# Kernel tuning notes

Hardware: AMD Instinct MI355X
Metric: run time of the kernel (lower is better)

The kernel has to match this reference:

```python
import jax, jax.numpy as jnp
import numpy as np

NUM_HEADS = 8
NUM_GROUPS = 32
EMB = 512
EPS = 1e-5


def setup_inputs() -> dict:
    key = jax.random.key(0)
    ks = jax.random.split(key, 12)
    B, C, H, W = 256, EMB, 16, 16
    s = 1.0 / np.sqrt(C)
    x = jax.random.normal(ks[0], (B, C, H, W), dtype=jnp.float32)
    Wq = jax.random.normal(ks[1], (C, EMB), dtype=jnp.float32) * s
    bq = jax.random.normal(ks[2], (EMB,), dtype=jnp.float32) * 0.01
    Wk = jax.random.normal(ks[3], (C, EMB), dtype=jnp.float32) * s
    bk = jax.random.normal(ks[4], (EMB,), dtype=jnp.float32) * 0.01
    Wv = jax.random.normal(ks[5], (C, EMB), dtype=jnp.float32) * s
    bv = jax.random.normal(ks[6], (EMB,), dtype=jnp.float32) * 0.01
    Wf = jax.random.normal(ks[7], (EMB, EMB), dtype=jnp.float32) * s
    bf = jax.random.normal(ks[8], (EMB,), dtype=jnp.float32) * 0.01
    gn_w = jnp.ones((EMB,), dtype=jnp.float32)
    gn_b = jnp.zeros((EMB,), dtype=jnp.float32)
    return {"x": x, "Wq": Wq, "bq": bq, "Wk": Wk, "bk": bk,
            "Wv": Wv, "bv": bv, "Wf": Wf, "bf": bf,
            "gn_w": gn_w, "gn_b": gn_b}


def reference(x, Wq, bq, Wk, bk, Wv, bv, Wf, bf, gn_w, gn_b):
    B, C, H, W = x.shape
    S = H * W
    nh = NUM_HEADS
    dh = EMB // nh
    xs = x.reshape(B, C, S).transpose(0, 2, 1)  # [B, S, C]
    q = (xs @ Wq + bq).reshape(B, S, nh, dh)
    k = (xs @ Wk + bk).reshape(B, S, nh, dh)
    v = (xs @ Wv + bv).reshape(B, S, nh, dh)
    scale = dh ** -0.5
    logits = jnp.einsum('bshd,bthd->bhst', q, k) * scale  # [B, nh, S, S]
    attn = jax.nn.softmax(logits, axis=-1)
    o = jnp.einsum('bhst,bthd->bshd', attn, v).reshape(B, S, EMB)
    o = o @ Wf + bf  # [B, S, EMB]
    y = o.transpose(0, 2, 1).reshape(B, EMB, H, W) + x  # residual
    # GroupNorm over (channels-within-group, H, W)
    G = NUM_GROUPS
    yg = y.reshape(B, G, EMB // G, H, W)
    mu = jnp.mean(yg, axis=(2, 3, 4), keepdims=True)
    var = jnp.var(yg, axis=(2, 3, 4), keepdims=True)
    yn = ((yg - mu) * jax.lax.rsqrt(var + EPS)).reshape(B, EMB, H, W)
    return yn * gn_w.reshape(1, EMB, 1, 1) + gn_b.reshape(1, EMB, 1, 1)
```

## Files before the change

kernel.cpp:

```cpp
#include <hip/hip_runtime.h>
#include <hip/hip_bf16.h>
#include <stdint.h>

#define B_  256
#define C_  512
#define S_  256
#define NH  8
#define DH  64

typedef float f32x4 __attribute__((ext_vector_type(4)));
typedef short s16x8 __attribute__((ext_vector_type(8)));

static __device__ __forceinline__ unsigned short f2bf(float f) {
  union { float f; unsigned u; } v; v.f = f;
  unsigned r = v.u + 0x7FFFu + ((v.u >> 16) & 1u);
  return (unsigned short)(r >> 16);
}

static __device__ __forceinline__ unsigned pk_bf16(float lo, float hi) {
  unsigned r;
  asm("v_cvt_pk_bf16_f32 %0, %1, %2" : "=v"(r) : "v"(lo), "v"(hi));
  return r;
}

static __device__ __forceinline__ void gload_lds16(const void* g, void* l) {
  __builtin_amdgcn_global_load_lds((const __attribute__((address_space(1))) void*)g,
                                   (__attribute__((address_space(3))) void*)l,
                                   16, 0, 0);
}

__global__ __launch_bounds__(256) void prep_w(const float* __restrict__ Wq,
                                              const float* __restrict__ Wk,
                                              const float* __restrict__ Wv,
                                              const float* __restrict__ Wf,
                                              unsigned short* __restrict__ Whead,
                                              unsigned short* __restrict__ Wft) {
  int mat = blockIdx.z;
  const float* src = (mat == 0) ? Wq : (mat == 1) ? Wk : (mat == 2) ? Wv : Wf;
  int n0 = blockIdx.x * 64, c0 = blockIdx.y * 64;
  __shared__ float tile[64][65];
  int t = threadIdx.x;
  int tr = t >> 4;
  int tc = (t & 15) * 4;
#pragma unroll
  for (int i = 0; i < 4; ++i) {
    int c = tr + i * 16;
    float4 v = *(const float4*)&src[(size_t)(c0 + c) * 512 + n0 + tc];
    tile[c][tc + 0] = v.x; tile[c][tc + 1] = v.y;
    tile[c][tc + 2] = v.z; tile[c][tc + 3] = v.w;
  }
  __syncthreads();
  int h = n0 >> 6;
  unsigned short* dst = (mat < 3) ? (Whead + ((size_t)h * 192 + mat * 64) * 512)
                                  : (Wft + (size_t)n0 * 512);
#pragma unroll
  for (int i = 0; i < 4; ++i) {
    int nl = tr + i * 16;
    ushort4 o;
    o.x = f2bf(tile[tc + 0][nl]); o.y = f2bf(tile[tc + 1][nl]);
    o.z = f2bf(tile[tc + 2][nl]); o.w = f2bf(tile[tc + 3][nl]);
    *(ushort4*)&dst[(size_t)nl * 512 + c0 + tc] = o;
  }
}

__global__ __launch_bounds__(256) void prep_x(const float* __restrict__ x,
                                              unsigned short* __restrict__ xs) {
  int b = blockIdx.z, s0 = blockIdx.x * 64, c0 = blockIdx.y * 64;
  __shared__ float tile[64][65];
  int t = threadIdx.x;
  int tr = t >> 4, tc = (t & 15) * 4;
  const float* xb = x + (size_t)b * C_ * S_;
#pragma unroll
  for (int i = 0; i < 4; ++i) {
    int c = tr + i * 16;
    float4 v = *(const float4*)&xb[(size_t)(c0 + c) * S_ + s0 + tc];
    tile[c][tc + 0] = v.x; tile[c][tc + 1] = v.y;
    tile[c][tc + 2] = v.z; tile[c][tc + 3] = v.w;
  }
  __syncthreads();
  unsigned short* xsb = xs + (size_t)b * S_ * C_;
#pragma unroll
  for (int i = 0; i < 4; ++i) {
    int s = tr + i * 16;
    ushort4 o;
    o.x = f2bf(tile[tc + 0][s]); o.y = f2bf(tile[tc + 1][s]);
    o.z = f2bf(tile[tc + 2][s]); o.w = f2bf(tile[tc + 3][s]);
    *(ushort4*)&xsb[(size_t)(s0 + s) * C_ + c0 + tc] = o;
  }
}

#define QKP 68
#define QOFF 0
#define KOFF 34816
#define VOFF 69632
__global__ __launch_bounds__(512) void qkvattn(const unsigned short* __restrict__ xs,
                                               const unsigned short* __restrict__ Whead,
                                               const float* __restrict__ bq,
                                               const float* __restrict__ bk,
                                               const float* __restrict__ bv,
                                               unsigned short* __restrict__ o) {
  __shared__ __align__(16) char lds[114688];
  int bid = blockIdx.x;
  int lin = (bid & 7) * 256 + (bid >> 3);
  int h = lin & 7, b = lin >> 3;
  int t = threadIdx.x, lane = t & 63, w = t >> 6;
  int l15 = lane & 15, l4 = lane >> 4;
  int wr = w >> 2, wc = w & 3;
  const unsigned short* xsb = xs + (size_t)b * S_ * C_;
  const unsigned short* wh  = Whead + (size_t)h * 192 * C_;

#define FSTAGE(kt, p)                                                         \
  {                                                                           \
    _Pragma("unroll")                                                         \
    for (int i = 0; i < 4; ++i) {                                             \
      int ch = i * 512 + t, r = ch >> 3, g = ch & 7;                          \
      int gs = g ^ (r & 7);                                                   \
      gload_lds16(xsb + (size_t)r * C_ + (kt) * 64 + gs * 8,                  \
                  lds + (p) * 57344 + ch * 16);                               \
    }                                                                         \
    _Pragma("unroll")                                                         \
    for (int i = 0; i < 3; ++i) {                                             \
      int ch = i * 512 + t, r = ch >> 3, g = ch & 7;                          \
      int gs = g ^ (r & 7);                                                   \
      gload_lds16(wh + (size_t)r * C_ + (kt) * 64 + gs * 8,                   \
                  lds + (p) * 57344 + 32768 + ch * 16);                       \
    }                                                                         \
  }

  f32x4 acc[8][3] = {};
  FSTAGE(0, 0);

  for (int kt = 0; kt < 8; ++kt) {
    if (kt < 7) FSTAGE(kt + 1, (kt + 1) & 1);
    if (kt < 7) asm volatile("s_waitcnt vmcnt(7)" ::: "memory");
    else        asm volatile("s_waitcnt vmcnt(0)" ::: "memory");
    __builtin_amdgcn_s_barrier();
    asm volatile("" ::: "memory");
    const char* Ab = lds + (kt & 1) * 57344;
    const char* Bb = Ab + 32768;
#pragma unroll
    for (int kk = 0; kk < 2; ++kk) {
      s16x8 afr[8], bfr[3];
#pragma unroll
      for (int fi = 0; fi < 8; ++fi) {
        int r = wr * 128 + fi * 16 + l15;
        afr[fi] = *(const s16x8*)(Ab + r * 128 + (((kk * 4 + l4) ^ (r & 7)) << 4));
      }
#pragma unroll
      for (int fj = 0; fj < 3; ++fj) {
        int r = wc * 48 + fj * 16 + l15;
        bfr[fj] = *(const s16x8*)(Bb + r * 128 + (((kk * 4 + l4) ^ (r & 7)) << 4));
      }
      __builtin_amdgcn_s_setprio(1);
#pragma unroll
      for (int fi = 0; fi < 8; ++fi)
#pragma unroll
        for (int fj = 0; fj < 3; ++fj)
          acc[fi][fj] = __builtin_amdgcn_mfma_f32_16x16x32_bf16(afr[fi], bfr[fj], acc[fi][fj], 0, 0, 0);
      __builtin_amdgcn_s_setprio(0);
    }
    __builtin_amdgcn_s_barrier();
  }
#undef FSTAGE

  unsigned short* Ql = (unsigned short*)(lds + QOFF);
  unsigned short* Kl = (unsigned short*)(lds + KOFF);
  unsigned short* Vl = (unsigned short*)(lds + VOFF);
  int h64 = h * 64;
#pragma unroll
  for (int fj = 0; fj < 3; ++fj) {
    int n = wc * 48 + fj * 16 + l15;
    int sel = n >> 6, d = n & 63;
    const float* bias = (sel == 0) ? bq : (sel == 1) ? bk : bv;
    float bias_v = bias[h64 + d];
    if (sel == 2) {
#pragma unroll
      for (int fi = 0; fi < 8; ++fi) {
        int s0 = wr * 128 + fi * 16 + l4 * 4;
        ushort4 o4;
        o4.x = f2bf(acc[fi][fj][0] + bias_v);
        o4.y = f2bf(acc[fi][fj][1] + bias_v);
        o4.z = f2bf(acc[fi][fj][2] + bias_v);
        o4.w = f2bf(acc[fi][fj][3] + bias_v);
        *(ushort4*)&Vl[d * 264 + s0] = o4;
      }
    } else {
      unsigned short* dstl = (sel == 0) ? Ql : Kl;
#pragma unroll
      for (int fi = 0; fi < 8; ++fi)
#pragma unroll
        for (int rg = 0; rg < 4; ++rg) {
          int s = wr * 128 + fi * 16 + l4 * 4 + rg;
          int row = s;
          if (sel == 1) {
            int s64 = s & 63, w32 = s64 & 31;
            row = (s & 192) + (s64 >> 5) * 32 + ((w32 >> 2) & 1) * 16 + (w32 >> 3) * 4 + (w32 & 3);
          }
          dstl[row * QKP + d] = f2bf(acc[fi][fj][rg] + bias_v);
        }
    }
  }
  __syncthreads();

  s16x8 qf[2][2];
#pragma unroll
  for (int fi = 0; fi < 2; ++fi)
#pragma unroll
    for (int kk = 0; kk < 2; ++kk) {
      int row = w * 32 + fi * 16 + l15;
      qf[fi][kk] = *(const s16x8*)((const char*)lds + QOFF + row * (QKP * 2) + kk * 64 + l4 * 16);
    }

  f32x4 acco[4][2] = {};
  float m_run[2] = {-3e38f, -3e38f}, l_run[2] = {0.f, 0.f};
  const float SCL = 0.125f * 1.44269504089f;

  for (int kb = 0; kb < 4; ++kb) {
    f32x4 accs[4][2] = {};
#pragma unroll
    for (int kk = 0; kk < 2; ++kk) {
      s16x8 kf[4];
#pragma unroll
      for (int fj = 0; fj < 4; ++fj)
        kf[fj] = *(const s16x8*)((const char*)lds + KOFF + (kb * 64 + fj * 16 + l15) * (QKP * 2) + kk * 64 + l4 * 16);
      __builtin_amdgcn_s_setprio(1);
#pragma unroll
      for (int fj = 0; fj < 4; ++fj)
#pragma unroll
        for (int fi = 0; fi < 2; ++fi)
          accs[fj][fi] = __builtin_amdgcn_mfma_f32_16x16x32_bf16(kf[fj], qf[fi][kk], accs[fj][fi], 0, 0, 0);
      __builtin_amdgcn_s_setprio(0);
    }
#pragma unroll
    for (int fi = 0; fi < 2; ++fi) {
      float m0[4];
#pragma unroll
      for (int fj = 0; fj < 4; ++fj)
        m0[fj] = fmaxf(fmaxf(accs[fj][fi][0], accs[fj][fi][1]),
                       fmaxf(accs[fj][fi][2], accs[fj][fi][3]));
      float mx = fmaxf(fmaxf(m0[0], m0[1]), fmaxf(m0[2], m0[3]));
      mx = fmaxf(mx, __shfl_xor(mx, 16, 64));
      mx = fmaxf(mx, __shfl_xor(mx, 32, 64));
      float mnew = fmaxf(m_run[fi], mx);
      float alpha = __builtin_amdgcn_exp2f((m_run[fi] - mnew) * SCL);
      m_run[fi] = mnew;
      float s0[4];
#pragma unroll
      for (int fj = 0; fj < 4; ++fj) {
#pragma unroll
        for (int rg = 0; rg < 4; ++rg) {
          float p = __builtin_amdgcn_exp2f((accs[fj][fi][rg] - mnew) * SCL);
          accs[fj][fi][rg] = p;
        }
        s0[fj] = (accs[fj][fi][0] + accs[fj][fi][1]) + (accs[fj][fi][2] + accs[fj][fi][3]);
      }
      float lsum = (s0[0] + s0[1]) + (s0[2] + s0[3]);
      lsum += __shfl_xor(lsum, 16, 64);
      lsum += __shfl_xor(lsum, 32, 64);
      l_run[fi] = l_run[fi] * alpha + lsum;
#pragma unroll
      for (int fd = 0; fd < 4; ++fd)
#pragma unroll
        for (int rg = 0; rg < 4; ++rg) acco[fd][fi][rg] *= alpha;
    }
#pragma unroll
    for (int kk2 = 0; kk2 < 2; ++kk2) {
      s16x8 vf[4];
#pragma unroll
      for (int fd = 0; fd < 4; ++fd)
        vf[fd] = *(const s16x8*)((const char*)lds + VOFF + (fd * 16 + l15) * 528 + kb * 128 + kk2 * 64 + l4 * 16);
#pragma unroll
      for (int fi = 0; fi < 2; ++fi) {
        union { unsigned u[4]; s16x8 v; } pb;
        pb.u[0] = pk_bf16(accs[2 * kk2][fi][0],     accs[2 * kk2][fi][1]);
        pb.u[1] = pk_bf16(accs[2 * kk2][fi][2],     accs[2 * kk2][fi][3]);
        pb.u[2] = pk_bf16(accs[2 * kk2 + 1][fi][0], accs[2 * kk2 + 1][fi][1]);
        pb.u[3] = pk_bf16(accs[2 * kk2 + 1][fi][2], accs[2 * kk2 + 1][fi][3]);
        __builtin_amdgcn_s_setprio(1);
#pragma unroll
        for (int fd = 0; fd < 4; ++fd)
          acco[fd][fi] = __builtin_amdgcn_mfma_f32_16x16x32_bf16(vf[fd], pb.v, acco[fd][fi], 0, 0, 0);
        __builtin_amdgcn_s_setprio(0);
      }
    }
  }

  unsigned short* ob = o + (size_t)b * S_ * C_ + h * DH;
#pragma unroll
  for (int fi = 0; fi < 2; ++fi) {
    float inv = 1.0f / l_run[fi];
    int qrow = w * 32 + fi * 16 + l15;
#pragma unroll
    for (int fd = 0; fd < 4; ++fd) {
      ushort4 s4;
      s4.x = f2bf(acco[fd][fi][0] * inv);
      s4.y = f2bf(acco[fd][fi][1] * inv);
      s4.z = f2bf(acco[fd][fi][2] * inv);
      s4.w = f2bf(acco[fd][fi][3] * inv);
      *(ushort4*)&ob[(size_t)qrow * C_ + fd * 16 + l4 * 4] = s4;
    }
  }
}

__global__ __launch_bounds__(512) void proj_gn(const unsigned short* __restrict__ o,
                                               const unsigned short* __restrict__ Wft,
                                               const float* __restrict__ bfp,
                                               const float* __restrict__ x,
                                               const float* __restrict__ gnw,
                                               const float* __restrict__ gnb,
                                               float* __restrict__ out) {
  __shared__ __align__(16) char plds[98304];
  __shared__ float red_s[128], red_q[128];
  __shared__ float mu_s[8], rs_s[8];
  int b = blockIdx.y, ct = blockIdx.x;
  int t = threadIdx.x, lane = t & 63, w = t >> 6;
  int l15 = lane & 15, l4 = lane >> 4;
  int wc = w >> 2, wsq = w & 3;
  if (t < 128) { red_s[t] = 0.f; red_q[t] = 0.f; }
  f32x4 acc[4][4] = {};
  const unsigned short* wt = Wft + (size_t)ct * 128 * C_;
  const unsigned short* ob = o + (size_t)b * S_ * C_;

#define PSTAGE(kt, p)                                                         \
  {                                                                           \
    _Pragma("unroll")                                                         \
    for (int i = 0; i < 2; ++i) {                                             \
      int ch = i * 512 + t, r = ch >> 3, g = ch & 7;                          \
      int gs = g ^ (r & 7);                                                   \
      gload_lds16(wt + (size_t)r * C_ + (kt) * 64 + gs * 8,                   \
                  plds + (p) * 49152 + ch * 16);                              \
    }                                                                         \
    _Pragma("unroll")                                                         \
    for (int i = 0; i < 4; ++i) {                                             \
      int ch = i * 512 + t, r = ch >> 3, g = ch & 7;                          \
      int gs = g ^ (r & 7);                                                   \
      gload_lds16(ob + (size_t)r * C_ + (kt) * 64 + gs * 8,                   \
                  plds + (p) * 49152 + 16384 + ch * 16);                      \
    }                                                                         \
  }

  PSTAGE(0, 0);

  for (int kt = 0; kt < 8; ++kt) {
    if (kt < 7) PSTAGE(kt + 1, (kt + 1) & 1);
    if (kt < 7) asm volatile("s_waitcnt vmcnt(6)" ::: "memory");
    else        asm volatile("s_waitcnt vmcnt(0)" ::: "memory");
    __builtin_amdgcn_s_barrier();
    asm volatile("" ::: "memory");
    const char* Ab = plds + (kt & 1) * 49152;
    const char* Bb = Ab + 16384;
#pragma unroll
    for (int kk = 0; kk < 2; ++kk) {
      s16x8 af[4], bfr[4];
#pragma unroll
      for (int fi = 0; fi < 4; ++fi) {
        int r = wc * 64 + fi * 16 + l15;
        af[fi] = *(const s16x8*)(Ab + r * 128 + (((kk * 4 + l4) ^ (r & 7)) << 4));
      }
#pragma unroll
      for (int fj = 0; fj < 4; ++fj) {
        int r = wsq * 64 + fj * 16 + l15;
        bfr[fj] = *(const s16x8*)(Bb + r * 128 + (((kk * 4 + l4) ^ (r & 7)) << 4));
      }
      __builtin_amdgcn_s_setprio(1);
#pragma unroll
      for (int fi = 0; fi < 4; ++fi)
#pragma unroll
        for (int fj = 0; fj < 4; ++fj)
          acc[fi][fj] = __builtin_amdgcn_mfma_f32_16x16x32_bf16(af[fi], bfr[fj], acc[fi][fj], 0, 0, 0);
      __builtin_amdgcn_s_setprio(0);
    }
    __builtin_amdgcn_s_barrier();
  }
#undef PSTAGE

  const float* xb = x + (size_t)b * C_ * S_;
  int c_base = ct * 128 + wc * 64;
  int s_base = wsq * 64;
#pragma unroll
  for (int fi = 0; fi < 4; ++fi)
#pragma unroll
    for (int rg = 0; rg < 4; ++rg) {
      int c = c_base + fi * 16 + l4 * 4 + rg;
      float bias_v = bfp[c];
      float psum = 0.f, psq = 0.f;
#pragma unroll
      for (int fj = 0; fj < 4; ++fj) {
        int s = s_base + fj * 16 + l15;
        float y = acc[fi][fj][rg] + bias_v + xb[(size_t)c * S_ + s];
        acc[fi][fj][rg] = y;
        psum += y; psq += y * y;
      }
#pragma unroll
      for (int off = 1; off < 16; off <<= 1) {
        psum += __shfl_xor(psum, off, 64);
        psq += __shfl_xor(psq, off, 64);
      }
      if (l15 == 0) {
        int cl = c - ct * 128;
        atomicAdd(&red_s[cl], psum);
        atomicAdd(&red_q[cl], psq);
      }
    }
  __syncthreads();
  if (t < 8) {
    float s = 0.f, qq = 0.f;
#pragma unroll
    for (int i = 0; i < 16; ++i) { s += red_s[t * 16 + i]; qq += red_q[t * 16 + i]; }
    float mu = s * (1.0f / 4096.0f);
    float var = qq * (1.0f / 4096.0f) - mu * mu;
    mu_s[t] = mu;
    rs_s[t] = rsqrtf(var + 1e-5f);
  }
  __syncthreads();
  float* outb = out + (size_t)b * C_ * S_;
#pragma unroll
  for (int fi = 0; fi < 4; ++fi)
#pragma unroll
    for (int rg = 0; rg < 4; ++rg) {
      int c = c_base + fi * 16 + l4 * 4 + rg;
      int gl = (c - ct * 128) >> 4;
      float mu = mu_s[gl], rs = rs_s[gl];
      float gw = gnw[c], gb = gnb[c];
#pragma unroll
      for (int fj = 0; fj < 4; ++fj) {
        int s = s_base + fj * 16 + l15;
        outb[(size_t)c * S_ + s] = (acc[fi][fj][rg] - mu) * rs * gw + gb;
      }
    }
}

extern "C" void kernel_launch(void* const* d_in, const int* in_sizes, int n_in,
                              void* d_out, int out_size, void* d_ws, size_t ws_size,
                              hipStream_t stream) {
  const float* x   = (const float*)d_in[0];
  const float* Wq  = (const float*)d_in[1];
  const float* bq  = (const float*)d_in[2];
  const float* Wk  = (const float*)d_in[3];
  const float* bk  = (const float*)d_in[4];
  const float* Wv  = (const float*)d_in[5];
  const float* bv  = (const float*)d_in[6];
  const float* Wf  = (const float*)d_in[7];
  const float* bf  = (const float*)d_in[8];
  const float* gnw = (const float*)d_in[9];
  const float* gnb = (const float*)d_in[10];

  char* ws = (char*)d_ws;
  unsigned short* Whead = (unsigned short*)ws;
  unsigned short* Wft   = (unsigned short*)(ws + 0x180000);
  unsigned short* xs    = (unsigned short*)(ws + 0x200000);
  unsigned short* obuf  = (unsigned short*)(ws + 0x200000 + (size_t)B_ * S_ * C_ * 2);
  float* out = (float*)d_out;

  hipLaunchKernelGGL(prep_w, dim3(8, 8, 4), dim3(256), 0, stream, Wq, Wk, Wv, Wf, Whead, Wft);
  hipLaunchKernelGGL(prep_x, dim3(4, 8, 256), dim3(256), 0, stream, x, xs);
  hipLaunchKernelGGL(qkvattn, dim3(2048), dim3(512), 0, stream,
                     xs, Whead, bq, bk, bv, obuf);
  hipLaunchKernelGGL(proj_gn, dim3(4, 256), dim3(512), 0, stream,
                     obuf, Wft, bf, x, gnw, gnb, out);
}
```

Baseline: 315.5 us.

## Shrink LDS footprint of fused QKV-attention kernel to allow two blocks per CU

Halves the K-step of the QKV projection pipeline (32 instead of 64 per stage, 16 iterations) so each double-buffered stage is smaller. Q is staged through LDS into registers first, then K overwrites the same region, so Q and K no longer need separate buffers. Total LDS drops from 112 KB to about 67 KB, which may let two 512-thread blocks share a CU. The cost is more loop iterations, extra barriers and a serialized Q-then-K epilogue.

```diff
diff --git a/kernel.cpp b/kernel.cpp
--- a/kernel.cpp
+++ b/kernel.cpp
@@ -90,16 +90,13 @@
 }
 
 #define QKP 68
-#define QOFF 0
-#define KOFF 34816
-#define VOFF 69632
 __global__ __launch_bounds__(512) void qkvattn(const unsigned short* __restrict__ xs,
                                                const unsigned short* __restrict__ Whead,
                                                const float* __restrict__ bq,
                                                const float* __restrict__ bk,
                                                const float* __restrict__ bv,
                                                unsigned short* __restrict__ o) {
-  __shared__ __align__(16) char lds[114688];
+  __shared__ __align__(16) char lds[68608];
   int bid = blockIdx.x;
   int lin = (bid & 7) * 256 + (bid >> 3);
   int h = lin & 7, b = lin >> 3;
@@ -112,104 +109,128 @@
 #define FSTAGE(kt, p)                                                         \
   {                                                                           \
     _Pragma("unroll")                                                         \
-    for (int i = 0; i < 4; ++i) {                                             \
-      int ch = i * 512 + t, r = ch >> 3, g = ch & 7;                          \
-      int gs = g ^ (r & 7);                                                   \
-      gload_lds16(xsb + (size_t)r * C_ + (kt) * 64 + gs * 8,                  \
-                  lds + (p) * 57344 + ch * 16);                               \
+    for (int i = 0; i < 2; ++i) {                                             \
+      int ch = i * 512 + t, r = ch >> 2, g = ch & 3;                          \
+      int gs = g ^ ((r >> 1) & 3);                                            \
+      gload_lds16(xsb + (size_t)r * C_ + (kt) * 32 + gs * 8,                  \
+                  lds + (p) * 28672 + ch * 16);                               \
     }                                                                         \
-    _Pragma("unroll")                                                         \
-    for (int i = 0; i < 3; ++i) {                                             \
-      int ch = i * 512 + t, r = ch >> 3, g = ch & 7;                          \
-      int gs = g ^ (r & 7);                                                   \
-      gload_lds16(wh + (size_t)r * C_ + (kt) * 64 + gs * 8,                   \
-                  lds + (p) * 57344 + 32768 + ch * 16);                       \
+    {                                                                         \
+      int ch = t, r = ch >> 2, g = ch & 3;                                    \
+      int gs = g ^ ((r >> 1) & 3);                                            \
+      gload_lds16(wh + (size_t)r * C_ + (kt) * 32 + gs * 8,                   \
+                  lds + (p) * 28672 + 16384 + ch * 16);                       \
+    }                                                                         \
+    if (t < 256) {                                                            \
+      int ch = 512 + t, r = ch >> 2, g = ch & 3;                              \
+      int gs = g ^ ((r >> 1) & 3);                                            \
+      gload_lds16(wh + (size_t)r * C_ + (kt) * 32 + gs * 8,                   \
+                  lds + (p) * 28672 + 16384 + ch * 16);                       \
     }                                                                         \
   }
 
   f32x4 acc[8][3] = {};
   FSTAGE(0, 0);
 
-  for (int kt = 0; kt < 8; ++kt) {
-    if (kt < 7) FSTAGE(kt + 1, (kt + 1) & 1);
-    if (kt < 7) asm volatile("s_waitcnt vmcnt(7)" ::: "memory");
-    else        asm volatile("s_waitcnt vmcnt(0)" ::: "memory");
+  for (int kt = 0; kt < 16; ++kt) {
+    if (kt < 15) {
+      FSTAGE(kt + 1, (kt + 1) & 1);
+      if (t < 256) asm volatile("s_waitcnt vmcnt(4)" ::: "memory");
+      else         asm volatile("s_waitcnt vmcnt(3)" ::: "memory");
+    } else {
+      asm volatile("s_waitcnt vmcnt(0)" ::: "memory");
+    }
     __builtin_amdgcn_s_barrier();
     asm volatile("" ::: "memory");
-    const char* Ab = lds + (kt & 1) * 57344;
-    const char* Bb = Ab + 32768;
-#pragma unroll
-    for (int kk = 0; kk < 2; ++kk) {
-      s16x8 afr[8], bfr[3];
-#pragma unroll
-      for (int fi = 0; fi < 8; ++fi) {
-        int r = wr * 128 + fi * 16 + l15;
-        afr[fi] = *(const s16x8*)(Ab + r * 128 + (((kk * 4 + l4) ^ (r & 7)) << 4));
-      }
-#pragma unroll
-      for (int fj = 0; fj < 3; ++fj) {
-        int r = wc * 48 + fj * 16 + l15;
-        bfr[fj] = *(const s16x8*)(Bb + r * 128 + (((kk * 4 + l4) ^ (r & 7)) << 4));
-      }
-      __builtin_amdgcn_s_setprio(1);
-#pragma unroll
-      for (int fi = 0; fi < 8; ++fi)
-#pragma unroll
-        for (int fj = 0; fj < 3; ++fj)
-          acc[fi][fj] = __builtin_amdgcn_mfma_f32_16x16x32_bf16(afr[fi], bfr[fj], acc[fi][fj], 0, 0, 0);
-      __builtin_amdgcn_s_setprio(0);
-    }
+    const char* Ab = lds + (kt & 1) * 28672;
+    const char* Bb = Ab + 16384;
+    s16x8 afr[8], bfr[3];
+#pragma unroll
+    for (int fi = 0; fi < 8; ++fi) {
+      int r = wr * 128 + fi * 16 + l15;
+      afr[fi] = *(const s16x8*)(Ab + r * 64 + ((l4 ^ ((r >> 1) & 3)) << 4));
+    }
+#pragma unroll
+    for (int fj = 0; fj < 3; ++fj) {
+      int r = wc * 48 + fj * 16 + l15;
+      bfr[fj] = *(const s16x8*)(Bb + r * 64 + ((l4 ^ ((r >> 1) & 3)) << 4));
+    }
+    __builtin_amdgcn_s_setprio(1);
+#pragma unroll
+    for (int fi = 0; fi < 8; ++fi)
+#pragma unroll
+      for (int fj = 0; fj < 3; ++fj)
+        acc[fi][fj] = __builtin_amdgcn_mfma_f32_16x16x32_bf16(afr[fi], bfr[fj], acc[fi][fj], 0, 0, 0);
+    __builtin_amdgcn_s_setprio(0);
     __builtin_amdgcn_s_barrier();
   }
 #undef FSTAGE
 
-  unsigned short* Ql = (unsigned short*)(lds + QOFF);
-  unsigned short* Kl = (unsigned short*)(lds + KOFF);
-  unsigned short* Vl = (unsigned short*)(lds + VOFF);
+  unsigned short* Qt = (unsigned short*)lds;
+  unsigned short* Vl = (unsigned short*)(lds + 34816);
   int h64 = h * 64;
+  float bv3[3];
 #pragma unroll
   for (int fj = 0; fj < 3; ++fj) {
     int n = wc * 48 + fj * 16 + l15;
     int sel = n >> 6, d = n & 63;
-    const float* bias = (sel == 0) ? bq : (sel == 1) ? bk : bv;
-    float bias_v = bias[h64 + d];
-    if (sel == 2) {
+    bv3[fj] = ((sel == 0) ? bq : (sel == 1) ? bk : bv)[h64 + d];
+  }
+#pragma unroll
+  for (int fj = 0; fj < 3; ++fj) {
+    int n = wc * 48 + fj * 16 + l15;
+    int sel = n >> 6, d = n & 63;
+    if (sel == 0) {
+#pragma unroll
+      for (int fi = 0; fi < 8; ++fi)
+#pragma unroll
+        for (int rg = 0; rg < 4; ++rg) {
+          int s = wr * 128 + fi * 16 + l4 * 4 + rg;
+          Qt[s * QKP + d] = f2bf(acc[fi][fj][rg] + bv3[fj]);
+        }
+    } else if (sel == 2) {
 #pragma unroll
       for (int fi = 0; fi < 8; ++fi) {
         int s0 = wr * 128 + fi * 16 + l4 * 4;
         ushort4 o4;
-        o4.x = f2bf(acc[fi][fj][0] + bias_v);
-        o4.y = f2bf(acc[fi][fj][1] + bias_v);
-        o4.z = f2bf(acc[fi][fj][2] + bias_v);
-        o4.w = f2bf(acc[fi][fj][3] + bias_v);
+        o4.x = f2bf(acc[fi][fj][0] + bv3[fj]);
+        o4.y = f2bf(acc[fi][fj][1] + bv3[fj]);
+        o4.z = f2bf(acc[fi][fj][2] + bv3[fj]);
+        o4.w = f2bf(acc[fi][fj][3] + bv3[fj]);
         *(ushort4*)&Vl[d * 264 + s0] = o4;
       }
-    } else {
-      unsigned short* dstl = (sel == 0) ? Ql : Kl;
+    }
+  }
+  __syncthreads();
+
+  s16x8 qf[2][2];
+#pragma unroll
+  for (int fi = 0; fi < 2; ++fi)
+#pragma unroll
+    for (int kk = 0; kk < 2; ++kk) {
+      int row = w * 32 + fi * 16 + l15;
+      qf[fi][kk] = *(const s16x8*)((const char*)lds + row * (QKP * 2) + kk * 64 + l4 * 16);
+    }
+  __syncthreads();
+
+  unsigned short* Kl = (unsigned short*)lds;
+#pragma unroll
+  for (int fj = 0; fj < 3; ++fj) {
+    int n = wc * 48 + fj * 16 + l15;
+    int sel = n >> 6, d = n & 63;
+    if (sel == 1) {
 #pragma unroll
       for (int fi = 0; fi < 8; ++fi)
 #pragma unroll
         for (int rg = 0; rg < 4; ++rg) {
           int s = wr * 128 + fi * 16 + l4 * 4 + rg;
-          int row = s;
-          if (sel == 1) {
-            int s64 = s & 63, w32 = s64 & 31;
-            row = (s & 192) + (s64 >> 5) * 32 + ((w32 >> 2) & 1) * 16 + (w32 >> 3) * 4 + (w32 & 3);
-          }
-          dstl[row * QKP + d] = f2bf(acc[fi][fj][rg] + bias_v);
+          int s64 = s & 63, w32 = s64 & 31;
+          int row = (s & 192) + (s64 >> 5) * 32 + ((w32 >> 2) & 1) * 16 + (w32 >> 3) * 4 + (w32 & 3);
+          Kl[row * QKP + d] = f2bf(acc[fi][fj][rg] + bv3[fj]);
         }
     }
   }
   __syncthreads();
-
-  s16x8 qf[2][2];
-#pragma unroll
-  for (int fi = 0; fi < 2; ++fi)
-#pragma unroll
-    for (int kk = 0; kk < 2; ++kk) {
-      int row = w * 32 + fi * 16 + l15;
-      qf[fi][kk] = *(const s16x8*)((const char*)lds + QOFF + row * (QKP * 2) + kk * 64 + l4 * 16);
-    }
 
   f32x4 acco[4][2] = {};
   float m_run[2] = {-3e38f, -3e38f}, l_run[2] = {0.f, 0.f};
@@ -222,7 +243,7 @@
       s16x8 kf[4];
 #pragma unroll
       for (int fj = 0; fj < 4; ++fj)
-        kf[fj] = *(const s16x8*)((const char*)lds + KOFF + (kb * 64 + fj * 16 + l15) * (QKP * 2) + kk * 64 + l4 * 16);
+        kf[fj] = *(const s16x8*)((const char*)lds + (kb * 64 + fj * 16 + l15) * (QKP * 2) + kk * 64 + l4 * 16);
       __builtin_amdgcn_s_setprio(1);
 #pragma unroll
       for (int fj = 0; fj < 4; ++fj)
@@ -268,7 +289,7 @@
       s16x8 vf[4];
 #pragma unroll
       for (int fd = 0; fd < 4; ++fd)
-        vf[fd] = *(const s16x8*)((const char*)lds + VOFF + (fd * 16 + l15) * 528 + kb * 128 + kk2 * 64 + l4 * 16);
+        vf[fd] = *(const s16x8*)((const char*)lds + 34816 + (fd * 16 + l15) * 528 + kb * 128 + kk2 * 64 + l4 * 16);
 #pragma unroll
       for (int fi = 0; fi < 2; ++fi) {
         union { unsigned u[4]; s16x8 v; } pb;
```

Result: slower. 327.2 us (+3.7%).
